# Optimization experiments

Measured on AMD Instinct MI355X. Metric: run time of the kernel, lower is better.

The kernel has to match this reference:

```python
import jax, jax.numpy as jnp
import numpy as np

N_FFTS = (64, 128, 256, 512)
SAMPLE_RATE = 2048
KERNEL_LENGTH = 8
T_SAMPLES = SAMPLE_RATE * KERNEL_LENGTH  # 16384


def _spec_shape(n_fft, n_samples):
    hop = n_fft // 2
    return (n_fft // 2 + 1, n_samples // hop + 1)


_SHAPES = [_spec_shape(n, T_SAMPLES) for n in N_FFTS]
NUM_FREQS = max(s[0] for s in _SHAPES)  # 257
NUM_TIMES = max(s[1] for s in _SHAPES)  # 513


def _spectrogram(x, n_fft):
    """torchaudio.transforms.Spectrogram(n_fft, normalized=True) equivalent.
    Defaults: win_length=n_fft, hop=n_fft//2, hann(periodic), center=True,
    reflect pad, onesided, power=2, normalized='window'.
    x: (..., T) -> (..., n_fft//2+1, n_frames)
    """
    hop = n_fft // 2
    n = jnp.arange(n_fft, dtype=x.dtype)
    w = 0.5 - 0.5 * jnp.cos(2.0 * jnp.pi * n / n_fft)  # periodic hann
    pad = n_fft // 2
    xp = jnp.pad(x, [(0, 0)] * (x.ndim - 1) + [(pad, pad)], mode='reflect')
    n_frames = 1 + (xp.shape[-1] - n_fft) // hop
    idx = hop * jnp.arange(n_frames)[:, None] + jnp.arange(n_fft)[None, :]
    frames = xp[..., idx] * w  # (..., n_frames, n_fft)
    spec = jnp.abs(jnp.fft.rfft(frames, axis=-1)) ** 2 / jnp.sum(w * w)
    return jnp.moveaxis(spec, -1, -2)  # (..., freq, time)


def setup_inputs() -> dict:
    key = jax.random.key(0)
    X = jax.random.normal(key, (64, 2, T_SAMPLES), dtype=jnp.float32)
    return {"X": X}


def reference(X):
    # Remap indices: int(i * shape / max_shape); gather directly from each
    # un-padded spec (indices are always in-range), then elementwise max.
    out = None
    for n_fft, (F_s, N_s) in zip(N_FFTS, _SHAPES):
        spec = _spectrogram(X, n_fft)  # (B, C, F_s, N_s)
        fidx = (jnp.arange(NUM_FREQS) * F_s) // NUM_FREQS  # (M,)
        tidx = (jnp.arange(NUM_TIMES) * N_s) // NUM_TIMES  # (N,)
        remapped = spec[..., fidx[:, None], tidx[None, :]]  # (B, C, M, N)
        out = remapped if out is None else jnp.maximum(out, remapped)
    return out
```

## Files before the change

kernel.cpp:

```cpp
#include <hip/hip_runtime.h>
#include <math.h>

#define T_SAMPLES 16384
#define BC 128
#define NUM_FREQS 257
#define NUM_TIMES 513

#define OFF0 0
#define OFF1 2166912
#define OFF2 4305152
#define OFF3 6435200

typedef float vf2 __attribute__((ext_vector_type(2)));
typedef float vf4 __attribute__((ext_vector_type(4)));
typedef vf4 vf4u __attribute__((aligned(4)));

__device__ inline vf2 cmul(vf2 a, vf2 b) {
    vf2 ar = { -a.y, a.x };
    return b.x * a + b.y * ar;
}

template <int LOGN, int P>
__device__ void fft_tile_body(const float* __restrict__ x, float* __restrict__ spec,
                              int tile, int bc, float* smem) {
    constexpr int N     = 1 << LOGN;
    constexpr int HOP   = N / 2;
    constexpr int F     = HOP + 1;
    constexpr int NT    = T_SAMPLES / HOP + 1;
    constexpr int NPAIR = (NT + 1) / 2;
    constexpr int R     = N / 64;
    constexpr int RS    = N + N / 32 + 2;
    const float NORM4   = 0.25f * 8.0f / (3.0f * (float)N);

    float* zre = smem;
    float* zim = smem + P * RS;

    const int tid   = threadIdx.x;
    const int lane  = tid & 63;
    const int wave  = tid >> 6;
    const int pair0 = tile * P;
    const int t0    = pair0 * 2;

    float sgn[6];
    vf2   twe[6];
#pragma unroll
    for (int b = 0; b < 6; ++b) {
        const bool hi = (lane >> b) & 1;
        float k = (float)(lane & ((1 << b) - 1));
        float s, c;
        sincosf(-2.0f * (float)M_PI * k / (float)(1 << (b + 1)), &s, &c);
        twe[b] = hi ? vf2{c, s} : vf2{1.0f, 0.0f};
        sgn[b] = hi ? -1.0f : 1.0f;
    }
    vf2 tw6 = {1,0}, tw7 = {1,0}, tw8 = {1,0};
    if constexpr (LOGN >= 7) { float s,c; sincosf(-2.0f*(float)M_PI*(float)lane/128.0f,&s,&c); tw6={c,s}; }
    if constexpr (LOGN >= 8) { float s,c; sincosf(-2.0f*(float)M_PI*(float)lane/256.0f,&s,&c); tw7={c,s}; }
    if constexpr (LOGN >= 9) { float s,c; sincosf(-2.0f*(float)M_PI*(float)lane/512.0f,&s,&c); tw8={c,s}; }

    float wr[R];
#pragma unroll
    for (int r = 0; r < R; ++r) {
        int n = r * 64 + lane;
        wr[r] = 0.5f - 0.5f * cosf(2.0f * (float)M_PI * (float)n / (float)N);
    }

    const float* xb = x + (size_t)bc * T_SAMPLES;

    constexpr int KLOOP = P / 4;
    for (int k2 = 0; k2 < KLOOP; ++k2) {
        const int p  = k2 * 4 + wave;
        const int pg = pair0 + p;
        if (pg < NPAIR) {
            const int t1 = 2 * pg, t2 = t1 + 1;
            vf2 d[R];

            const bool refl = (t1 == 0) || (t1 * HOP + N - 1 >= T_SAMPLES) || (t2 >= NT);
            if (!refl) {
                const float* src = xb + t1 * HOP - HOP;
#pragma unroll
                for (int r = 0; r < R; ++r) {
                    int n = r * 64 + lane;
                    vf2 v = { src[n], src[n + HOP] };
                    d[r] = v * wr[r];
                }
            } else {
#pragma unroll
                for (int r = 0; r < R; ++r) {
                    int n = r * 64 + lane;
                    int g = t1 * HOP + n - HOP;
                    g = (g < 0) ? -g : g;
                    g = (g >= T_SAMPLES) ? (2 * T_SAMPLES - 2 - g) : g;
                    float re = xb[g] * wr[r];
                    float im = 0.0f;
                    if (t2 < NT) {
                        int h = t2 * HOP + n - HOP;
                        h = (h < 0) ? -h : h;
                        h = (h >= T_SAMPLES) ? (2 * T_SAMPLES - 2 - h) : h;
                        im = xb[h] * wr[r];
                    }
                    d[r] = { re, im };
                }
            }

            if constexpr (LOGN >= 9) {
                const vf2 u8 = { 0.70710678118654752f, -0.70710678118654752f };
                vf2 tt = tw8;
#pragma unroll
                for (int r = 0; r < 4; ++r) {
                    vf2 a = d[r], b = d[r + 4];
                    d[r]     = a + b;
                    d[r + 4] = cmul(a - b, tt);
                    tt = cmul(tt, u8);
                }
            }
            if constexpr (LOGN >= 8) {
                const vf2 t0_ = tw7;
                const vf2 t1_ = { tw7.y, -tw7.x };
#pragma unroll
                for (int g = 0; g < R; g += 4) {
                    { vf2 a = d[g],   b = d[g+2]; d[g]   = a + b; d[g+2] = cmul(a - b, t0_); }
                    { vf2 a = d[g+1], b = d[g+3]; d[g+1] = a + b; d[g+3] = cmul(a - b, t1_); }
                }
            }
            if constexpr (LOGN >= 7) {
#pragma unroll
                for (int g = 0; g < R; g += 2) {
                    vf2 a = d[g], b = d[g+1];
                    d[g]   = a + b;
                    d[g+1] = cmul(a - b, tw6);
                }
            }

#pragma unroll
            for (int b = 5; b >= 1; --b) {
                const int   mask = 1 << b;
                const vf2   w    = twe[b];
                const float s    = sgn[b];
#pragma unroll
                for (int r = 0; r < R; ++r) {
                    vf2 p2;
                    p2.x = __shfl_xor(d[r].x, mask, 64);
                    p2.y = __shfl_xor(d[r].y, mask, 64);
                    vf2 t  = p2 + d[r] * s;
                    vf2 tr = { -t.y, t.x };
                    d[r] = w.x * t + w.y * tr;
                }
            }
            {
                const float s = sgn[0];
#pragma unroll
                for (int r = 0; r < R; ++r) {
                    vf2 p2;
                    p2.x = __shfl_xor(d[r].x, 1, 64);
                    p2.y = __shfl_xor(d[r].y, 1, 64);
                    d[r] = p2 + d[r] * s;
                }
            }

#pragma unroll
            for (int r = 0; r < R; ++r) {
                int idx = r * 64 + lane;
                int f   = (int)(__brev((unsigned)idx) >> (32 - LOGN));
                int pos = p * RS + f + (f >> 5);
                zre[pos] = d[r].x;
                zim[pos] = d[r].y;
            }
        }
    }
    __syncthreads();

    float* sbase = spec + (size_t)bc * F * NT;
    for (int e = tid; e < F * P; e += 256) {
        int f = e / P;
        int p = e % P;
        int t = t0 + 2 * p;
        if (t < NT) {
            int fn = (N - f) & (N - 1);
            int pa = p * RS + f  + (f  >> 5);
            int pb = p * RS + fn + (fn >> 5);
            float ax = zre[pa], ay = zim[pa];
            float bx = zre[pb], by = zim[pb];
            float rx = ax + bx, ry = ay - by;
            sbase[(size_t)f * NT + t] = (rx * rx + ry * ry) * NORM4;
            if (t + 1 < NT) {
                float sx = ax - bx, sy = ay + by;
                sbase[(size_t)f * NT + t + 1] = (sx * sx + sy * sy) * NORM4;
            }
        }
    }
}

__global__ __launch_bounds__(256) void fft_all_kernel(const float* __restrict__ x,
                                                      float* __restrict__ ws) {
    __shared__ float smem[4256];
    const int bx = blockIdx.x;
    const int bc = blockIdx.y;
    if (bx < 33)       fft_tile_body<6, 8>(x, ws + OFF0, bx,      bc, smem);
    else if (bx < 50)  fft_tile_body<7, 8>(x, ws + OFF1, bx - 33, bc, smem);
    else if (bx < 59)  fft_tile_body<8, 8>(x, ws + OFF2, bx - 50, bc, smem);
    else               fft_tile_body<9, 4>(x, ws + OFF3, bx - 59, bc, smem);
}

__global__ __launch_bounds__(256) void remap_max_kernel(const float* __restrict__ ws,
                                                        float* __restrict__ out) {
    const int JG    = 129;
    const int total = BC * NUM_FREQS * JG;
    int idx = blockIdx.x * 256 + threadIdx.x;
    if (idx >= total) return;
    int jg  = idx % JG;
    int rem = idx / JG;
    int i   = rem % NUM_FREQS;
    int bc  = rem / NUM_FREQS;
    int j0  = jg * 4;
    const bool full = (j0 + 3 < NUM_TIMES);

    float mv[4];
    {
        int fi = (i * 33) / NUM_FREQS;
        const float* p = ws + OFF0 + ((size_t)bc * 33 + fi) * 513 + j0;
        if (full) {
            vf4 v = *(const vf4u*)p;
            mv[0] = v.x; mv[1] = v.y; mv[2] = v.z; mv[3] = v.w;
        } else {
            mv[0] = p[0]; mv[1] = mv[2] = mv[3] = 0.0f;
        }
    }
#pragma unroll
    for (int k = 0; k < 4; ++k) {
        int j = j0 + k;
        if (j < NUM_TIMES) {
#define GATHER(OFF, F_, NT_)                                                   \
            {                                                                  \
                int fi = (i * F_) / NUM_FREQS;                                 \
                int ti = (j * NT_) / NUM_TIMES;                                \
                float v = ws[(size_t)(OFF) + ((size_t)bc * (F_) + fi) * (NT_) + ti]; \
                mv[k] = fmaxf(mv[k], v);                                       \
            }
            GATHER(OFF1, 65, 257)
            GATHER(OFF2, 129, 129)
            GATHER(OFF3, 257, 65)
#undef GATHER
        }
    }

    float* po = out + ((size_t)bc * NUM_FREQS + i) * NUM_TIMES + j0;
    if (full) {
        vf4 v = { mv[0], mv[1], mv[2], mv[3] };
        *(vf4u*)po = v;
    } else {
        po[0] = mv[0];
    }
}

extern "C" void kernel_launch(void* const* d_in, const int* in_sizes, int n_in,
                              void* d_out, int out_size, void* d_ws, size_t ws_size,
                              hipStream_t stream) {
    const float* x = (const float*)d_in[0];
    float* ws  = (float*)d_ws;
    float* out = (float*)d_out;

    fft_all_kernel<<<dim3(68, BC), 256, 0, stream>>>(x, ws);

    const int total = BC * NUM_FREQS * 129;
    remap_max_kernel<<<(total + 255) / 256, 256, 0, stream>>>(ws, out);
}
```

Baseline: 136.2 us.

## Batch FFT frames per wave, use DPP for short butterflies, rebalance tiles

Each wave now holds several frame pairs in registers at once and runs every butterfly stage across all of them, which exposes instruction-level parallelism and cuts loop overhead. The two shortest-distance butterfly stages use DPP lane swizzles in place of ds_bpermute-based shuffles. The small FFT sizes get larger tiles, so the grid shrinks from 68 to 36 blocks per channel, and the LDS row stride and shared-memory size are adjusted. In exchange, register pressure rises and the number of blocks in the grid falls.

```diff
diff --git a/kernel.cpp b/kernel.cpp
--- a/kernel.cpp
+++ b/kernel.cpp
@@ -18,6 +18,13 @@
 __device__ inline vf2 cmul(vf2 a, vf2 b) {
     vf2 ar = { -a.y, a.x };
     return b.x * a + b.y * ar;
+}
+
+template <int CTRL>
+__device__ inline float dppf(float x) {
+    return __builtin_bit_cast(float,
+        __builtin_amdgcn_update_dpp(0, __builtin_bit_cast(int, x),
+                                    CTRL, 0xF, 0xF, true));
 }
 
 template <int LOGN, int P>
@@ -29,7 +36,8 @@
     constexpr int NT    = T_SAMPLES / HOP + 1;
     constexpr int NPAIR = (NT + 1) / 2;
     constexpr int R     = N / 64;
-    constexpr int RS    = N + N / 32 + 2;
+    constexpr int RS    = N + N / 32 + 1;
+    constexpr int KLOOP = P / 4;
     const float NORM4   = 0.25f * 8.0f / (3.0f * (float)N);
 
     float* zre = smem;
@@ -66,14 +74,16 @@
 
     const float* xb = x + (size_t)bc * T_SAMPLES;
 
-    constexpr int KLOOP = P / 4;
-    for (int k2 = 0; k2 < KLOOP; ++k2) {
-        const int p  = k2 * 4 + wave;
+    vf2  d[KLOOP][R];
+    bool act[KLOOP];
+
+#pragma unroll
+    for (int q = 0; q < KLOOP; ++q) {
+        const int p  = q * 4 + wave;
         const int pg = pair0 + p;
-        if (pg < NPAIR) {
+        act[q] = (pg < NPAIR);
+        if (act[q]) {
             const int t1 = 2 * pg, t2 = t1 + 1;
-            vf2 d[R];
-
             const bool refl = (t1 == 0) || (t1 * HOP + N - 1 >= T_SAMPLES) || (t2 >= NT);
             if (!refl) {
                 const float* src = xb + t1 * HOP - HOP;
@@ -81,7 +91,7 @@
                 for (int r = 0; r < R; ++r) {
                     int n = r * 64 + lane;
                     vf2 v = { src[n], src[n + HOP] };
-                    d[r] = v * wr[r];
+                    d[q][r] = v * wr[r];
                 }
             } else {
 #pragma unroll
@@ -98,72 +108,108 @@
                         h = (h >= T_SAMPLES) ? (2 * T_SAMPLES - 2 - h) : h;
                         im = xb[h] * wr[r];
                     }
-                    d[r] = { re, im };
+                    d[q][r] = { re, im };
                 }
             }
-
-            if constexpr (LOGN >= 9) {
-                const vf2 u8 = { 0.70710678118654752f, -0.70710678118654752f };
-                vf2 tt = tw8;
-#pragma unroll
-                for (int r = 0; r < 4; ++r) {
-                    vf2 a = d[r], b = d[r + 4];
-                    d[r]     = a + b;
-                    d[r + 4] = cmul(a - b, tt);
-                    tt = cmul(tt, u8);
-                }
-            }
-            if constexpr (LOGN >= 8) {
-                const vf2 t0_ = tw7;
-                const vf2 t1_ = { tw7.y, -tw7.x };
-#pragma unroll
-                for (int g = 0; g < R; g += 4) {
-                    { vf2 a = d[g],   b = d[g+2]; d[g]   = a + b; d[g+2] = cmul(a - b, t0_); }
-                    { vf2 a = d[g+1], b = d[g+3]; d[g+1] = a + b; d[g+3] = cmul(a - b, t1_); }
-                }
-            }
-            if constexpr (LOGN >= 7) {
-#pragma unroll
-                for (int g = 0; g < R; g += 2) {
-                    vf2 a = d[g], b = d[g+1];
-                    d[g]   = a + b;
-                    d[g+1] = cmul(a - b, tw6);
-                }
-            }
-
-#pragma unroll
-            for (int b = 5; b >= 1; --b) {
-                const int   mask = 1 << b;
-                const vf2   w    = twe[b];
-                const float s    = sgn[b];
-#pragma unroll
-                for (int r = 0; r < R; ++r) {
-                    vf2 p2;
-                    p2.x = __shfl_xor(d[r].x, mask, 64);
-                    p2.y = __shfl_xor(d[r].y, mask, 64);
-                    vf2 t  = p2 + d[r] * s;
-                    vf2 tr = { -t.y, t.x };
-                    d[r] = w.x * t + w.y * tr;
-                }
-            }
-            {
-                const float s = sgn[0];
-#pragma unroll
-                for (int r = 0; r < R; ++r) {
-                    vf2 p2;
-                    p2.x = __shfl_xor(d[r].x, 1, 64);
-                    p2.y = __shfl_xor(d[r].y, 1, 64);
-                    d[r] = p2 + d[r] * s;
-                }
-            }
-
+        } else {
+#pragma unroll
+            for (int r = 0; r < R; ++r) d[q][r] = vf2{0.0f, 0.0f};
+        }
+    }
+
+    if constexpr (LOGN >= 9) {
+        const vf2 u8 = { 0.70710678118654752f, -0.70710678118654752f };
+#pragma unroll
+        for (int q = 0; q < KLOOP; ++q) {
+            vf2 tt = tw8;
+#pragma unroll
+            for (int r = 0; r < 4; ++r) {
+                vf2 a = d[q][r], b = d[q][r + 4];
+                d[q][r]     = a + b;
+                d[q][r + 4] = cmul(a - b, tt);
+                tt = cmul(tt, u8);
+            }
+        }
+    }
+    if constexpr (LOGN >= 8) {
+        const vf2 t0_ = tw7;
+        const vf2 t1_ = { tw7.y, -tw7.x };
+#pragma unroll
+        for (int q = 0; q < KLOOP; ++q) {
+#pragma unroll
+            for (int g = 0; g < R; g += 4) {
+                { vf2 a = d[q][g],   b = d[q][g+2]; d[q][g]   = a + b; d[q][g+2] = cmul(a - b, t0_); }
+                { vf2 a = d[q][g+1], b = d[q][g+3]; d[q][g+1] = a + b; d[q][g+3] = cmul(a - b, t1_); }
+            }
+        }
+    }
+    if constexpr (LOGN >= 7) {
+#pragma unroll
+        for (int q = 0; q < KLOOP; ++q) {
+#pragma unroll
+            for (int g = 0; g < R; g += 2) {
+                vf2 a = d[q][g], b = d[q][g+1];
+                d[q][g]   = a + b;
+                d[q][g+1] = cmul(a - b, tw6);
+            }
+        }
+    }
+
+#pragma unroll
+    for (int b = 5; b >= 2; --b) {
+        const int   mask = 1 << b;
+        const vf2   w    = twe[b];
+        const float s    = sgn[b];
+#pragma unroll
+        for (int q = 0; q < KLOOP; ++q) {
+#pragma unroll
+            for (int r = 0; r < R; ++r) {
+                vf2 p2;
+                p2.x = __shfl_xor(d[q][r].x, mask, 64);
+                p2.y = __shfl_xor(d[q][r].y, mask, 64);
+                vf2 t  = p2 + d[q][r] * s;
+                vf2 tr = { -t.y, t.x };
+                d[q][r] = w.x * t + w.y * tr;
+            }
+        }
+    }
+    {
+        const vf2   w = twe[1];
+        const float s = sgn[1];
+#pragma unroll
+        for (int q = 0; q < KLOOP; ++q) {
+#pragma unroll
+            for (int r = 0; r < R; ++r) {
+                vf2 p2 = { dppf<0x4E>(d[q][r].x), dppf<0x4E>(d[q][r].y) };
+                vf2 t  = p2 + d[q][r] * s;
+                vf2 tr = { -t.y, t.x };
+                d[q][r] = w.x * t + w.y * tr;
+            }
+        }
+    }
+    {
+        const float s = sgn[0];
+#pragma unroll
+        for (int q = 0; q < KLOOP; ++q) {
+#pragma unroll
+            for (int r = 0; r < R; ++r) {
+                vf2 p2 = { dppf<0xB1>(d[q][r].x), dppf<0xB1>(d[q][r].y) };
+                d[q][r] = p2 + d[q][r] * s;
+            }
+        }
+    }
+
+#pragma unroll
+    for (int q = 0; q < KLOOP; ++q) {
+        if (act[q]) {
+            const int p = q * 4 + wave;
 #pragma unroll
             for (int r = 0; r < R; ++r) {
                 int idx = r * 64 + lane;
                 int f   = (int)(__brev((unsigned)idx) >> (32 - LOGN));
                 int pos = p * RS + f + (f >> 5);
-                zre[pos] = d[r].x;
-                zim[pos] = d[r].y;
+                zre[pos] = d[q][r].x;
+                zim[pos] = d[q][r].y;
             }
         }
     }
@@ -192,13 +238,13 @@
 
 __global__ __launch_bounds__(256) void fft_all_kernel(const float* __restrict__ x,
                                                       float* __restrict__ ws) {
-    __shared__ float smem[4256];
+    __shared__ float smem[4288];
     const int bx = blockIdx.x;
     const int bc = blockIdx.y;
-    if (bx < 33)       fft_tile_body<6, 8>(x, ws + OFF0, bx,      bc, smem);
-    else if (bx < 50)  fft_tile_body<7, 8>(x, ws + OFF1, bx - 33, bc, smem);
-    else if (bx < 59)  fft_tile_body<8, 8>(x, ws + OFF2, bx - 50, bc, smem);
-    else               fft_tile_body<9, 4>(x, ws + OFF3, bx - 59, bc, smem);
+    if (bx < 9)        fft_tile_body<6, 32>(x, ws + OFF0, bx,      bc, smem);
+    else if (bx < 18)  fft_tile_body<7, 16>(x, ws + OFF1, bx - 9,  bc, smem);
+    else if (bx < 27)  fft_tile_body<8, 8> (x, ws + OFF2, bx - 18, bc, smem);
+    else               fft_tile_body<9, 4> (x, ws + OFF3, bx - 27, bc, smem);
 }
 
 __global__ __launch_bounds__(256) void remap_max_kernel(const float* __restrict__ ws,
@@ -259,7 +305,7 @@
     float* ws  = (float*)d_ws;
     float* out = (float*)d_out;
 
-    fft_all_kernel<<<dim3(68, BC), 256, 0, stream>>>(x, ws);
+    fft_all_kernel<<<dim3(36, BC), 256, 0, stream>>>(x, ws);
 
     const int total = BC * NUM_FREQS * 129;
     remap_max_kernel<<<(total + 255) / 256, 256, 0, stream>>>(ws, out);
```

Result: faster. 128.9 us (-5.3%).
